# Kernel tuning notes

Measured on AMD Instinct MI355X. Metric: run time of the kernel, lower is better.

## Reference

```python
import jax, jax.numpy as jnp
import numpy as np

D_MODEL = 1024
NUM_TILES = 64
TPC = 8                 # tiles per cluster
NC = NUM_TILES // TPC   # num clusters = 8
GRID = 16
CH = D_MODEL // 4       # compress hidden = 256
EPS_LN = 1e-5


def setup_inputs() -> dict:
    key = jax.random.key(0)
    ks = jax.random.split(key, 8)
    B, T = 8, 4096
    x = jax.random.normal(ks[0], (B, T, D_MODEL), dtype=jnp.float32)
    gamma = jnp.ones((D_MODEL,), jnp.float32)
    beta = jnp.zeros((D_MODEL,), jnp.float32)
    W1 = jax.random.normal(ks[1], (CH, D_MODEL), jnp.float32) * 0.02
    b1 = jnp.zeros((CH,), jnp.float32)
    W2 = jax.random.normal(ks[2], (2, CH), jnp.float32) * 0.02
    b2 = jnp.zeros((2,), jnp.float32)
    spline_coeffs = jax.random.normal(ks[3], (NUM_TILES, GRID, GRID, 3), jnp.float32) * 0.5
    spline_scales = jnp.ones((NUM_TILES,), jnp.float32)
    directions = jax.random.normal(ks[4], (NUM_TILES, D_MODEL), jnp.float32) * 0.02
    output_scale = jnp.ones((), jnp.float32) * 0.1
    return {"x": x, "gamma": gamma, "beta": beta, "W1": W1, "b1": b1,
            "W2": W2, "b2": b2, "spline_coeffs": spline_coeffs,
            "spline_scales": spline_scales, "directions": directions,
            "output_scale": output_scale}


def _forward(x, gamma, beta, W1, b1, W2, b2, spline_coeffs, spline_scales,
             directions, output_scale):
    B, T, D = x.shape
    N = B * T
    # LayerNorm
    mu = jnp.mean(x, axis=-1, keepdims=True)
    var = jnp.mean((x - mu) ** 2, axis=-1, keepdims=True)
    x_norm = (x - mu) / jnp.sqrt(var + EPS_LN) * gamma + beta
    xf = x_norm.reshape(N, D)

    # routing signatures
    sigs = jnp.sign(directions)                                  # [NT, D]
    cluster_sigs = jnp.sign(sigs.reshape(NC, TPC, D).mean(axis=1))  # [NC, D]

    # hierarchical routing: cluster argmax then tile argmax within cluster
    cluster_idx = jnp.argmax(xf @ cluster_sigs.T, axis=-1)       # [N]
    tile_scores = (xf @ sigs.T).reshape(N, NC, TPC)              # [N, NC, TPC]
    sel = jnp.take_along_axis(tile_scores, cluster_idx[:, None, None], axis=1)[:, 0, :]
    local_idx = jnp.argmax(sel, axis=-1)                         # [N]
    tile_idx = cluster_idx * TPC + local_idx                     # cluster tiles are contiguous

    # shared compression -> (a, b) in [-1, 1]
    h = jax.nn.gelu(xf @ W1.T + b1, approximate=False)
    comp = jnp.tanh(h @ W2.T + b2)                               # [N, 2]
    a, b = comp[:, 0], comp[:, 1]

    # ternary quantized spline coefficients (STE forward value)
    q = jnp.where(spline_coeffs > 0.3, 1.0,
                  jnp.where(spline_coeffs < -0.3, -1.0, 0.0))
    qc = spline_coeffs + jax.lax.stop_gradient(q - spline_coeffs)  # [NT, G, G, 3]

    idx_a = jnp.clip(((a + 1) / 2 * GRID).astype(jnp.int32), 0, GRID - 1)
    idx_b = jnp.clip(((b + 1) / 2 * GRID).astype(jnp.int32), 0, GRID - 1)
    cell = qc[tile_idx, idx_a, idx_b]                            # [N, 3]
    cell_size = 2.0 / GRID
    local_a = (a + 1 - idx_a.astype(jnp.float32) * cell_size) / cell_size
    local_b = (b + 1 - idx_b.astype(jnp.float32) * cell_size) / cell_size
    spline_val = cell[:, 0] + cell[:, 1] * local_a + cell[:, 2] * local_b
    scale_val = spline_val * spline_scales[tile_idx]             # [N]

    out = scale_val[:, None] * directions[tile_idx]              # [N, D]
    out = out.reshape(B, T, D) * output_scale
    output = x + out                                             # dropout is identity in eval

    # load-balance aux loss
    counts = jax.ops.segment_sum(jnp.ones((N,), jnp.float32), tile_idx,
                                 num_segments=NUM_TILES)
    ideal = N / NUM_TILES
    balance = jnp.mean((counts - ideal) ** 2) / (ideal ** 2 + 1e-8) * 0.01
    return output, tile_idx.reshape(B, T), comp.reshape(B, T, 2), balance


def reference(x, gamma, beta, W1, b1, W2, b2, spline_coeffs, spline_scales,
              directions, output_scale):
    return _forward(x, gamma, beta, W1, b1, W2, b2, spline_coeffs,
                    spline_scales, directions, output_scale)
```

## Files before the change

kernel.cpp:

```cpp
#include <hip/hip_runtime.h>

#define D_MODEL 1024
#define ROWS    32
#define BT      1024
#define EPS_LN  1e-5f

typedef _Float16 f16x8 __attribute__((ext_vector_type(8)));
typedef _Float16 f16x4 __attribute__((ext_vector_type(4)));
typedef float    f32x4 __attribute__((ext_vector_type(4)));

#define WS_CNT   0
#define WS_B1P   256
#define WS_CT    1280
#define WS_FH    4096
#define WS_FL    (4096 + 688128)
#define WS_NEED  (4096 + 2 * 688128)


__global__ void prep_kernel(const float* __restrict__ W1,
                            const float* __restrict__ dirs,
                            const float* __restrict__ gamma,
                            const float* __restrict__ beta,
                            const float* __restrict__ b1,
                            char* __restrict__ wsb, int useT) {
    const int b = blockIdx.x, tid = threadIdx.x;
    if (b < 168) {
        if (!useT) return;
        const int gid = b * 256 + tid;
        const int ct = gid >> 11, ks = (gid >> 6) & 31, l = gid & 63;
        const int c16 = l & 15, kb = ks * 32 + ((l >> 4) << 3);
        f16x8 h, lo;
#pragma unroll
        for (int i = 0; i < 8; ++i) {
            const int k = kb + i;
            const float g = gamma[k];
            float v;
            if (ct < 16) {
                v = g * W1[(ct * 16 + c16) * 1024 + k];
            } else if (ct < 20) {
                const float d = dirs[((ct - 16) * 16 + c16) * 1024 + k];
                v = g * (float)((d > 0.f) - (d < 0.f));
            } else {
                if (c16 < 8) {
                    int s = 0;
                    for (int t = 0; t < 8; ++t) {
                        const float d = dirs[(c16 * 8 + t) * 1024 + k];
                        s += (d > 0.f) - (d < 0.f);
                    }
                    v = g * (float)((s > 0) - (s < 0));
                } else v = 0.f;
            }
            const _Float16 hh = (_Float16)v;
            h[i] = hh; lo[i] = (_Float16)(v - (float)hh);
        }
        *(f16x8*)(wsb + WS_FH + (size_t)gid * 16) = h;
        *(f16x8*)(wsb + WS_FL + (size_t)gid * 16) = lo;
    } else if (b < 184) {
        __shared__ float red[256];
        const int jl = tid >> 4, sub = tid & 15;
        const int j = (b - 168) * 16 + jl;
        float s = 0.f;
        for (int i = 0; i < 64; ++i) {
            const int k = sub * 64 + i;
            s += beta[k] * W1[j * 1024 + k];
        }
        red[tid] = s;
        __syncthreads();
        if (sub == 0) {
            float t = 0.f;
            for (int p = 0; p < 16; ++p) t += red[jl * 16 + p];
            ((float*)(wsb + WS_B1P))[j] = b1[j] + t;
        }
    } else if (b < 192) {
        const int t8 = (b - 184) * 8 + (tid >> 5), l32 = tid & 31;
        float s = 0.f;
        for (int i = 0; i < 32; ++i) {
            const int k = l32 * 32 + i;
            const float d = dirs[t8 * 1024 + k];
            s += beta[k] * (float)((d > 0.f) - (d < 0.f));
        }
        s += __shfl_xor(s, 1); s += __shfl_xor(s, 2); s += __shfl_xor(s, 4);
        s += __shfl_xor(s, 8); s += __shfl_xor(s, 16);
        if (l32 == 0) ((float*)(wsb + WS_CT))[t8] = s;
    } else if (b == 192) {
        const int c = tid >> 5, l32 = tid & 31;
        float s = 0.f;
        for (int i = 0; i < 32; ++i) {
            const int k = l32 * 32 + i;
            int ss = 0;
            for (int t = 0; t < 8; ++t) {
                const float d = dirs[(c * 8 + t) * 1024 + k];
                ss += (d > 0.f) - (d < 0.f);
            }
            s += beta[k] * (float)((ss > 0) - (ss < 0));
        }
        s += __shfl_xor(s, 1); s += __shfl_xor(s, 2); s += __shfl_xor(s, 4);
        s += __shfl_xor(s, 8); s += __shfl_xor(s, 16);
        if (l32 == 0) ((float*)(wsb + WS_CT))[64 + c] = s;
    } else {
        if (tid < 64) ((unsigned*)(wsb + WS_CNT))[tid] = 0u;
        else if (tid < 72) ((float*)(wsb + WS_CT))[72 + (tid - 64)] = 0.f;
    }
}

template <int USET, int NT, int CT0>
__device__ __forceinline__ void loadB(const char* __restrict__ wsb,
                                      const float* __restrict__ W1,
                                      const float* __restrict__ dirs,
                                      const float* __restrict__ gamma,
                                      int ks, int ln, f16x8* bh, f16x8* bl) {
    if (USET) {
        const size_t fo = ((size_t)((CT0 * 32 + ks) * 64 + ln)) * 16;
#pragma unroll
        for (int t = 0; t < NT; ++t) {
            bh[t] = *(const f16x8*)(wsb + WS_FH + fo + (size_t)t * 32 * 64 * 16);
            bl[t] = *(const f16x8*)(wsb + WS_FL + fo + (size_t)t * 32 * 64 * 16);
        }
    } else {
        const int c16 = ln & 15, kb = ks * 32 + ((ln >> 4) << 3);
        float g[8];
#pragma unroll
        for (int i = 0; i < 8; ++i) g[i] = gamma[kb + i];
#pragma unroll
        for (int t = 0; t < NT; ++t) {
            const int ct = CT0 + t;
#pragma unroll
            for (int i = 0; i < 8; ++i) {
                const int k = kb + i;
                float v;
                if (ct < 16) {
                    v = g[i] * W1[(ct * 16 + c16) * 1024 + k];
                } else if (ct < 20) {
                    const float d = dirs[((ct - 16) * 16 + c16) * 1024 + k];
                    v = g[i] * (float)((d > 0.f) - (d < 0.f));
                } else {
                    if (c16 < 8) {
                        int s = 0;
                        for (int tt = 0; tt < 8; ++tt) {
                            const float d = dirs[(c16 * 8 + tt) * 1024 + k];
                            s += (d > 0.f) - (d < 0.f);
                        }
                        v = g[i] * (float)((s > 0) - (s < 0));
                    } else v = 0.f;
                }
                const _Float16 hh = (_Float16)v;
                bh[t][i] = hh; bl[t][i] = (_Float16)(v - (float)hh);
            }
        }
    }
}

template <int NT>
__device__ __forceinline__ void mfma6(const f16x8 (&a)[2][2], const f16x8* bh,
                                      const f16x8* bl, f32x4 (*acc)[2]) {
    __builtin_amdgcn_s_setprio(1);
#pragma unroll
    for (int t = 0; t < NT; ++t) {
        acc[t][0] = __builtin_amdgcn_mfma_f32_16x16x32_f16(a[0][0], bh[t], acc[t][0], 0, 0, 0);
        acc[t][1] = __builtin_amdgcn_mfma_f32_16x16x32_f16(a[1][0], bh[t], acc[t][1], 0, 0, 0);
    }
#pragma unroll
    for (int t = 0; t < NT; ++t) {
        acc[t][0] = __builtin_amdgcn_mfma_f32_16x16x32_f16(a[0][0], bl[t], acc[t][0], 0, 0, 0);
        acc[t][1] = __builtin_amdgcn_mfma_f32_16x16x32_f16(a[1][0], bl[t], acc[t][1], 0, 0, 0);
    }
#pragma unroll
    for (int t = 0; t < NT; ++t) {
        acc[t][0] = __builtin_amdgcn_mfma_f32_16x16x32_f16(a[0][1], bh[t], acc[t][0], 0, 0, 0);
        acc[t][1] = __builtin_amdgcn_mfma_f32_16x16x32_f16(a[1][1], bh[t], acc[t][1], 0, 0, 0);
    }
    __builtin_amdgcn_s_setprio(0);
}

template <int USET, int NT, int CT0>
__device__ __forceinline__ void runM(const _Float16* __restrict__ xh,
                                     const _Float16* __restrict__ xl,
                                     const char* __restrict__ wsb,
                                     const float* __restrict__ W1,
                                     const float* __restrict__ dirs,
                                     const float* __restrict__ gamma,
                                     const float* __restrict__ W2,
                                     int wv, int ln,
                                     float (*scores)[84], float (*part)[32][2]) {
    const int r16 = ln & 15, kgrp = ln >> 4;
    const int kofs = kgrp << 3, asw = (r16 & 7) << 3;
    const float* b1p = (const float*)(wsb + WS_B1P);
    const float* ctv = (const float*)(wsb + WS_CT);

    f32x4 acc[NT][2];
#pragma unroll
    for (int t = 0; t < NT; ++t) {
        acc[t][0] = (f32x4){0.f, 0.f, 0.f, 0.f};
        acc[t][1] = (f32x4){0.f, 0.f, 0.f, 0.f};
    }
    f16x8 bh0[NT], bl0[NT], bh1[NT], bl1[NT];
    f16x8 a0[2][2], a1[2][2];

#define LDA2(KS, A) { const int cc_ = (((KS) * 32 + kofs) ^ asw); \
                      const int i0_ = r16 * 1024 + cc_, i1_ = (16 + r16) * 1024 + cc_; \
                      A[0][0] = *(const f16x8*)&xh[i0_]; A[0][1] = *(const f16x8*)&xl[i0_]; \
                      A[1][0] = *(const f16x8*)&xh[i1_]; A[1][1] = *(const f16x8*)&xl[i1_]; }

    loadB<USET, NT, CT0>(wsb, W1, dirs, gamma, 0, ln, bh0, bl0);
    LDA2(0, a0);
    for (int ks = 0; ks < 32; ks += 2) {
        loadB<USET, NT, CT0>(wsb, W1, dirs, gamma, ks + 1, ln, bh1, bl1);
        LDA2(ks + 1, a1);
        mfma6<NT>(a0, bh0, bl0, acc);
        if (ks + 2 < 32) {
            loadB<USET, NT, CT0>(wsb, W1, dirs, gamma, ks + 2, ln, bh0, bl0);
            LDA2(ks + 2, a0);
        }
        mfma6<NT>(a1, bh1, bl1, acc);
    }
#undef LDA2

    float p0s[2][4] = {{0.f,0.f,0.f,0.f},{0.f,0.f,0.f,0.f}};
    float p1s[2][4] = {{0.f,0.f,0.f,0.f},{0.f,0.f,0.f,0.f}};
#pragma unroll
    for (int t = 0; t < NT; ++t) {
        const int ct = CT0 + t;
        if (ct < 16) {
            const int col = ct * 16 + r16;
            const float b1c = b1p[col], w20 = W2[col], w21 = W2[256 + col];
#pragma unroll
            for (int rt = 0; rt < 2; ++rt)
#pragma unroll
                for (int reg = 0; reg < 4; ++reg) {
                    const float h = acc[t][rt][reg] + b1c;
                    const float gl = 0.5f * h * (1.f + erff(h * 0.70710678118654752f));
                    p0s[rt][reg] += gl * w20; p1s[rt][reg] += gl * w21;
                }
        } else {
            const int sc = (ct - 16) * 16 + r16;
            const float cadd = ctv[sc];
#pragma unroll
            for (int rt = 0; rt < 2; ++rt)
#pragma unroll
                for (int reg = 0; reg < 4; ++reg)
                    scores[rt * 16 + kgrp * 4 + reg][sc] = acc[t][rt][reg] + cadd;
        }
    }
    if (CT0 < 16) {
#pragma unroll
        for (int rt = 0; rt < 2; ++rt)
#pragma unroll
            for (int reg = 0; reg < 4; ++reg) {
                float v0 = p0s[rt][reg], v1 = p1s[rt][reg];
                v0 += __shfl_xor(v0, 1); v0 += __shfl_xor(v0, 2);
                v0 += __shfl_xor(v0, 4); v0 += __shfl_xor(v0, 8);
                v1 += __shfl_xor(v1, 1); v1 += __shfl_xor(v1, 2);
                v1 += __shfl_xor(v1, 4); v1 += __shfl_xor(v1, 8);
                if (r16 == 0) {
                    const int row = rt * 16 + kgrp * 4 + reg;
                    part[wv][row][0] = v0; part[wv][row][1] = v1;
                }
            }
    }
}

template <int USET>
__launch_bounds__(BT, 1)
__global__ void main_kernel(const float* __restrict__ x,
                            const float* __restrict__ gamma,
                            const float* __restrict__ beta,
                            const float* __restrict__ W1,
                            const float* __restrict__ b1,
                            const float* __restrict__ W2,
                            const float* __restrict__ b2,
                            const float* __restrict__ spline,
                            const float* __restrict__ sscale,
                            const float* __restrict__ dirs,
                            const float* __restrict__ oscale,
                            float* __restrict__ out,
                            float* __restrict__ out_tile,
                            float* __restrict__ out_comp,
                            char* __restrict__ wsb) {
    __shared__ __align__(16) _Float16 xh[ROWS * 1024];
    __shared__ __align__(16) _Float16 xl[ROWS * 1024];
    __shared__ float scores[ROWS][84];
    __shared__ float part[16][ROWS][2];
    __shared__ float mu_s[ROWS], sstd_s[ROWS];
    __shared__ float comp_ab[ROWS][2], sval_s[ROWS];
    __shared__ int   tidx_s[ROWS];

    const int tid = threadIdx.x, wv = tid >> 6, ln = tid & 63;
    const int row0 = blockIdx.x * ROWS;

    for (int q = 0; q < 2; ++q) {
        const int rl = wv * 2 + q;
        const float4* xp = (const float4*)(x + (size_t)(row0 + rl) * D_MODEL);
        float4 xv[4];
        float s = 0.f;
#pragma unroll
        for (int i = 0; i < 4; ++i) {
            xv[i] = xp[ln + 64 * i];
            s += xv[i].x + xv[i].y + xv[i].z + xv[i].w;
        }
#pragma unroll
        for (int o = 1; o < 64; o <<= 1) s += __shfl_xor(s, o);
        const float mu = s * (1.f / 1024.f);
        float v = 0.f;
#pragma unroll
        for (int i = 0; i < 4; ++i) {
            float dx;
            dx = xv[i].x - mu; v += dx * dx;
            dx = xv[i].y - mu; v += dx * dx;
            dx = xv[i].z - mu; v += dx * dx;
            dx = xv[i].w - mu; v += dx * dx;
        }
#pragma unroll
        for (int o = 1; o < 64; o <<= 1) v += __shfl_xor(v, o);
        const float sstd = sqrtf(v * (1.f / 1024.f) + EPS_LN);
        const float rstd = 1.f / sstd;
        if (ln == 0) { mu_s[rl] = mu; sstd_s[rl] = sstd; }
        const int sw = (rl & 7) << 3;
#pragma unroll
        for (int i = 0; i < 4; ++i) {
            const float o0 = (xv[i].x - mu) * rstd, o1 = (xv[i].y - mu) * rstd;
            const float o2 = (xv[i].z - mu) * rstd, o3 = (xv[i].w - mu) * rstd;
            f16x4 hv, lv;
            _Float16 t0 = (_Float16)o0; hv[0] = t0; lv[0] = (_Float16)(o0 - (float)t0);
            _Float16 t1 = (_Float16)o1; hv[1] = t1; lv[1] = (_Float16)(o1 - (float)t1);
            _Float16 t2 = (_Float16)o2; hv[2] = t2; lv[2] = (_Float16)(o2 - (float)t2);
            _Float16 t3 = (_Float16)o3; hv[3] = t3; lv[3] = (_Float16)(o3 - (float)t3);
            const int k0 = 4 * (ln + 64 * i);
            const int idx = rl * 1024 + (k0 ^ sw);
            *(f16x4*)&xh[idx] = hv;
            *(f16x4*)&xl[idx] = lv;
        }
    }
    __syncthreads();

    if (wv == 0)       runM<USET, 2, 0 >(xh, xl, wsb, W1, dirs, gamma, W2, wv, ln, scores, part);
    else if (wv == 1)  runM<USET, 2, 2 >(xh, xl, wsb, W1, dirs, gamma, W2, wv, ln, scores, part);
    else if (wv == 2)  runM<USET, 2, 4 >(xh, xl, wsb, W1, dirs, gamma, W2, wv, ln, scores, part);
    else if (wv == 3)  runM<USET, 2, 6 >(xh, xl, wsb, W1, dirs, gamma, W2, wv, ln, scores, part);
    else if (wv == 4)  runM<USET, 2, 8 >(xh, xl, wsb, W1, dirs, gamma, W2, wv, ln, scores, part);
    else if (wv == 5)  runM<USET, 1, 10>(xh, xl, wsb, W1, dirs, gamma, W2, wv, ln, scores, part);
    else if (wv == 6)  runM<USET, 1, 11>(xh, xl, wsb, W1, dirs, gamma, W2, wv, ln, scores, part);
    else if (wv == 7)  runM<USET, 1, 12>(xh, xl, wsb, W1, dirs, gamma, W2, wv, ln, scores, part);
    else if (wv == 8)  runM<USET, 1, 13>(xh, xl, wsb, W1, dirs, gamma, W2, wv, ln, scores, part);
    else if (wv == 9)  runM<USET, 1, 14>(xh, xl, wsb, W1, dirs, gamma, W2, wv, ln, scores, part);
    else if (wv == 10) runM<USET, 1, 15>(xh, xl, wsb, W1, dirs, gamma, W2, wv, ln, scores, part);
    else if (wv == 11) runM<USET, 1, 16>(xh, xl, wsb, W1, dirs, gamma, W2, wv, ln, scores, part);
    else if (wv == 12) runM<USET, 1, 17>(xh, xl, wsb, W1, dirs, gamma, W2, wv, ln, scores, part);
    else if (wv == 13) runM<USET, 1, 18>(xh, xl, wsb, W1, dirs, gamma, W2, wv, ln, scores, part);
    else if (wv == 14) runM<USET, 1, 19>(xh, xl, wsb, W1, dirs, gamma, W2, wv, ln, scores, part);
    else               runM<USET, 1, 20>(xh, xl, wsb, W1, dirs, gamma, W2, wv, ln, scores, part);
    __syncthreads();

    unsigned* cntp = (unsigned*)(wsb + WS_CNT);
    if (tid < ROWS) {
        const int r = tid;
        int bc = 0; float bs = scores[r][64];
#pragma unroll
        for (int c = 1; c < 8; ++c) { const float v = scores[r][64 + c]; if (v > bs) { bs = v; bc = c; } }
        int bt = 0; float ts = scores[r][bc * 8];
#pragma unroll
        for (int p = 1; p < 8; ++p) { const float v = scores[r][bc * 8 + p]; if (v > ts) { ts = v; bt = p; } }
        const int ti = bc * 8 + bt;
        tidx_s[r] = ti;
        atomicAdd(&cntp[ti], 1u);
        out_tile[row0 + r] = (float)ti;
    } else if (tid >= 64 && tid < 64 + 2 * ROWS) {
        const int r = (tid - 64) >> 1, cc = tid & 1;
        float s = b2[cc];
#pragma unroll
        for (int w = 0; w < 11; ++w) s += part[w][r][cc];
        s = tanhf(s);
        comp_ab[r][cc] = s;
        out_comp[(size_t)(row0 + r) * 2 + cc] = s;
    }
    __syncthreads();

    if (tid < ROWS) {
        const int r = tid;
        const float a = comp_ab[r][0], b = comp_ab[r][1];
        int ia = (int)((a + 1.0f) / 2.0f * 16.0f);
        int ib = (int)((b + 1.0f) / 2.0f * 16.0f);
        ia = min(max(ia, 0), 15); ib = min(max(ib, 0), 15);
        const int ti = tidx_s[r];
        const float* cp = spline + ((ti * 16 + ia) * 16 + ib) * 3;
        float c0 = cp[0], c1 = cp[1], c2 = cp[2];
        c0 = (c0 > 0.3f) ? 1.f : ((c0 < -0.3f) ? -1.f : 0.f);
        c1 = (c1 > 0.3f) ? 1.f : ((c1 < -0.3f) ? -1.f : 0.f);
        c2 = (c2 > 0.3f) ? 1.f : ((c2 < -0.3f) ? -1.f : 0.f);
        const float la = (a + 1.0f - (float)ia * 0.125f) * 8.0f;
        const float lb = (b + 1.0f - (float)ib * 0.125f) * 8.0f;
        sval_s[r] = (c0 + c1 * la + c2 * lb) * sscale[ti];
    }
    __syncthreads();

    const float os = oscale[0];
    for (int q = 0; q < 2; ++q) {
        const int rl = wv * 2 + q, row = row0 + rl;
        const int ti = tidx_s[rl];
        const float s = sval_s[rl] * os;
        const float mu = mu_s[rl], sd = sstd_s[rl];
        const int sw = (rl & 7) << 3;
        const float4* dp = (const float4*)(dirs + (size_t)ti * D_MODEL);
        float4* op = (float4*)(out + (size_t)row * D_MODEL);
#pragma unroll
        for (int i = 0; i < 4; ++i) {
            const int k0 = 4 * (ln + 64 * i);
            const int idx = rl * 1024 + (k0 ^ sw);
            const f16x4 hv = *(const f16x4*)&xh[idx];
            const f16x4 lv = *(const f16x4*)&xl[idx];
            const float4 dv = dp[ln + 64 * i];
            float4 o4;
            o4.x = ((float)hv[0] + (float)lv[0]) * sd + mu + s * dv.x;
            o4.y = ((float)hv[1] + (float)lv[1]) * sd + mu + s * dv.y;
            o4.z = ((float)hv[2] + (float)lv[2]) * sd + mu + s * dv.z;
            o4.w = ((float)hv[3] + (float)lv[3]) * sd + mu + s * dv.w;
            op[ln + 64 * i] = o4;
        }
    }
}

__global__ void bal_kernel(const unsigned* __restrict__ counts, float* __restrict__ ob) {
    const int t = threadIdx.x;
    const float d = (float)counts[t] - 512.0f;
    float v = d * d;
#pragma unroll
    for (int o = 1; o < 64; o <<= 1) v += __shfl_xor(v, o);
    if (t == 0) ob[0] = (v * (1.f / 64.f)) / 262144.0f * 0.01f;
}

extern "C" void kernel_launch(void* const* d_in, const int* in_sizes, int n_in,
                              void* d_out, int out_size, void* d_ws, size_t ws_size,
                              hipStream_t stream) {
    const float* x      = (const float*)d_in[0];
    const float* gamma  = (const float*)d_in[1];
    const float* beta   = (const float*)d_in[2];
    const float* W1     = (const float*)d_in[3];
    const float* b1     = (const float*)d_in[4];
    const float* W2     = (const float*)d_in[5];
    const float* b2     = (const float*)d_in[6];
    const float* spline = (const float*)d_in[7];
    const float* sscale = (const float*)d_in[8];
    const float* dirs   = (const float*)d_in[9];
    const float* oscale = (const float*)d_in[10];

    const int nrows = in_sizes[0] / D_MODEL;
    float* out      = (float*)d_out;
    float* out_tile = out + (size_t)nrows * D_MODEL;
    float* out_comp = out_tile + nrows;
    float* out_bal  = out_comp + (size_t)nrows * 2;

    char* wsb = (char*)d_ws;
    const int useT = (ws_size >= (size_t)WS_NEED) ? 1 : 0;

    prep_kernel<<<194, 256, 0, stream>>>(W1, dirs, gamma, beta, b1, wsb, useT);
    if (useT)
        main_kernel<1><<<nrows / ROWS, BT, 0, stream>>>(x, gamma, beta, W1, b1, W2, b2,
                                                        spline, sscale, dirs, oscale,
                                                        out, out_tile, out_comp, wsb);
    else
        main_kernel<0><<<nrows / ROWS, BT, 0, stream>>>(x, gamma, beta, W1, b1, W2, b2,
                                                        spline, sscale, dirs, oscale,
                                                        out, out_tile, out_comp, wsb);
    bal_kernel<<<1, 64, 0, stream>>>((const unsigned*)(wsb + WS_CNT), out_bal);
}
```

Measured before the change: 174.3 us.

## Split GEMM waves into W1 and routing-score paths, use single-precision B for signs

The fused MFMA path is split into two variants. Waves computing W1 columns keep the 3-pass split-fp16 product, while the routing-score waves use a single fp16 B operand, since sign*gamma values are exact in fp16. This cuts the score waves from six MFMAs per step to four and drops their low-part B loads. It also moves the tanh compression step into the routing thread to remove one block barrier, and widens LDS accesses in the layernorm and output phases to 8-wide fp16 vectors. The score waves were not the slowest waves (NT=2 W1 waves dominate), so the critical path may not shrink much.

```diff
diff --git a/kernel.cpp b/kernel.cpp
--- a/kernel.cpp
+++ b/kernel.cpp
@@ -6,7 +6,6 @@
 #define EPS_LN  1e-5f
 
 typedef _Float16 f16x8 __attribute__((ext_vector_type(8)));
-typedef _Float16 f16x4 __attribute__((ext_vector_type(4)));
 typedef float    f32x4 __attribute__((ext_vector_type(4)));
 
 #define WS_CNT   0
@@ -104,11 +103,10 @@
 }
 
 template <int USET, int NT, int CT0>
-__device__ __forceinline__ void loadB(const char* __restrict__ wsb,
-                                      const float* __restrict__ W1,
-                                      const float* __restrict__ dirs,
-                                      const float* __restrict__ gamma,
-                                      int ks, int ln, f16x8* bh, f16x8* bl) {
+__device__ __forceinline__ void loadBW(const char* __restrict__ wsb,
+                                       const float* __restrict__ W1,
+                                       const float* __restrict__ gamma,
+                                       int ks, int ln, f16x8* bh, f16x8* bl) {
     if (USET) {
         const size_t fo = ((size_t)((CT0 * 32 + ks) * 64 + ln)) * 16;
 #pragma unroll
@@ -118,31 +116,12 @@
         }
     } else {
         const int c16 = ln & 15, kb = ks * 32 + ((ln >> 4) << 3);
-        float g[8];
-#pragma unroll
-        for (int i = 0; i < 8; ++i) g[i] = gamma[kb + i];
 #pragma unroll
         for (int t = 0; t < NT; ++t) {
-            const int ct = CT0 + t;
 #pragma unroll
             for (int i = 0; i < 8; ++i) {
                 const int k = kb + i;
-                float v;
-                if (ct < 16) {
-                    v = g[i] * W1[(ct * 16 + c16) * 1024 + k];
-                } else if (ct < 20) {
-                    const float d = dirs[((ct - 16) * 16 + c16) * 1024 + k];
-                    v = g[i] * (float)((d > 0.f) - (d < 0.f));
-                } else {
-                    if (c16 < 8) {
-                        int s = 0;
-                        for (int tt = 0; tt < 8; ++tt) {
-                            const float d = dirs[(c16 * 8 + tt) * 1024 + k];
-                            s += (d > 0.f) - (d < 0.f);
-                        }
-                        v = g[i] * (float)((s > 0) - (s < 0));
-                    } else v = 0.f;
-                }
+                const float v = gamma[k] * W1[((CT0 + t) * 16 + c16) * 1024 + k];
                 const _Float16 hh = (_Float16)v;
                 bh[t][i] = hh; bl[t][i] = (_Float16)(v - (float)hh);
             }
@@ -150,9 +129,41 @@
     }
 }
 
+template <int USET, int CT0>
+__device__ __forceinline__ f16x8 loadBS(const char* __restrict__ wsb,
+                                        const float* __restrict__ dirs,
+                                        const float* __restrict__ gamma,
+                                        int ks, int ln) {
+    if (USET) {
+        return *(const f16x8*)(wsb + WS_FH + ((size_t)((CT0 * 32 + ks) * 64 + ln)) * 16);
+    }
+    const int c16 = ln & 15, kb = ks * 32 + ((ln >> 4) << 3);
+    f16x8 s;
+#pragma unroll
+    for (int i = 0; i < 8; ++i) {
+        const int k = kb + i;
+        float v;
+        if (CT0 < 20) {
+            const float d = dirs[((CT0 - 16) * 16 + c16) * 1024 + k];
+            v = gamma[k] * (float)((d > 0.f) - (d < 0.f));
+        } else {
+            if (c16 < 8) {
+                int ss = 0;
+                for (int tt = 0; tt < 8; ++tt) {
+                    const float d = dirs[(c16 * 8 + tt) * 1024 + k];
+                    ss += (d > 0.f) - (d < 0.f);
+                }
+                v = gamma[k] * (float)((ss > 0) - (ss < 0));
+            } else v = 0.f;
+        }
+        s[i] = (_Float16)v;
+    }
+    return s;
+}
+
 template <int NT>
-__device__ __forceinline__ void mfma6(const f16x8 (&a)[2][2], const f16x8* bh,
-                                      const f16x8* bl, f32x4 (*acc)[2]) {
+__device__ __forceinline__ void mfma3p(const f16x8 (&a)[2][2], const f16x8* bh,
+                                       const f16x8* bl, f32x4 (*acc)[2]) {
     __builtin_amdgcn_s_setprio(1);
 #pragma unroll
     for (int t = 0; t < NT; ++t) {
@@ -171,92 +182,124 @@
     }
     __builtin_amdgcn_s_setprio(0);
 }
-
-template <int USET, int NT, int CT0>
-__device__ __forceinline__ void runM(const _Float16* __restrict__ xh,
-                                     const _Float16* __restrict__ xl,
-                                     const char* __restrict__ wsb,
-                                     const float* __restrict__ W1,
-                                     const float* __restrict__ dirs,
-                                     const float* __restrict__ gamma,
-                                     const float* __restrict__ W2,
-                                     int wv, int ln,
-                                     float (*scores)[84], float (*part)[32][2]) {
-    const int r16 = ln & 15, kgrp = ln >> 4;
-    const int kofs = kgrp << 3, asw = (r16 & 7) << 3;
-    const float* b1p = (const float*)(wsb + WS_B1P);
-    const float* ctv = (const float*)(wsb + WS_CT);
-
-    f32x4 acc[NT][2];
-#pragma unroll
-    for (int t = 0; t < NT; ++t) {
-        acc[t][0] = (f32x4){0.f, 0.f, 0.f, 0.f};
-        acc[t][1] = (f32x4){0.f, 0.f, 0.f, 0.f};
-    }
-    f16x8 bh0[NT], bl0[NT], bh1[NT], bl1[NT];
-    f16x8 a0[2][2], a1[2][2];
 
 #define LDA2(KS, A) { const int cc_ = (((KS) * 32 + kofs) ^ asw); \
                       const int i0_ = r16 * 1024 + cc_, i1_ = (16 + r16) * 1024 + cc_; \
                       A[0][0] = *(const f16x8*)&xh[i0_]; A[0][1] = *(const f16x8*)&xl[i0_]; \
                       A[1][0] = *(const f16x8*)&xh[i1_]; A[1][1] = *(const f16x8*)&xl[i1_]; }
 
-    loadB<USET, NT, CT0>(wsb, W1, dirs, gamma, 0, ln, bh0, bl0);
+template <int USET, int NT, int CT0>
+__device__ __forceinline__ void runW(const _Float16* __restrict__ xh,
+                                     const _Float16* __restrict__ xl,
+                                     const char* __restrict__ wsb,
+                                     const float* __restrict__ W1,
+                                     const float* __restrict__ gamma,
+                                     const float* __restrict__ W2,
+                                     int wv, int ln, float (*part)[32][2]) {
+    const int r16 = ln & 15, kgrp = ln >> 4;
+    const int kofs = kgrp << 3, asw = (r16 & 7) << 3;
+    const float* b1p = (const float*)(wsb + WS_B1P);
+
+    f32x4 acc[NT][2];
+#pragma unroll
+    for (int t = 0; t < NT; ++t) {
+        acc[t][0] = (f32x4){0.f, 0.f, 0.f, 0.f};
+        acc[t][1] = (f32x4){0.f, 0.f, 0.f, 0.f};
+    }
+    f16x8 bh0[NT], bl0[NT], bh1[NT], bl1[NT];
+    f16x8 a0[2][2], a1[2][2];
+
+    loadBW<USET, NT, CT0>(wsb, W1, gamma, 0, ln, bh0, bl0);
     LDA2(0, a0);
     for (int ks = 0; ks < 32; ks += 2) {
-        loadB<USET, NT, CT0>(wsb, W1, dirs, gamma, ks + 1, ln, bh1, bl1);
+        loadBW<USET, NT, CT0>(wsb, W1, gamma, ks + 1, ln, bh1, bl1);
         LDA2(ks + 1, a1);
-        mfma6<NT>(a0, bh0, bl0, acc);
+        mfma3p<NT>(a0, bh0, bl0, acc);
         if (ks + 2 < 32) {
-            loadB<USET, NT, CT0>(wsb, W1, dirs, gamma, ks + 2, ln, bh0, bl0);
+            loadBW<USET, NT, CT0>(wsb, W1, gamma, ks + 2, ln, bh0, bl0);
             LDA2(ks + 2, a0);
         }
-        mfma6<NT>(a1, bh1, bl1, acc);
-    }
-#undef LDA2
+        mfma3p<NT>(a1, bh1, bl1, acc);
+    }
 
     float p0s[2][4] = {{0.f,0.f,0.f,0.f},{0.f,0.f,0.f,0.f}};
     float p1s[2][4] = {{0.f,0.f,0.f,0.f},{0.f,0.f,0.f,0.f}};
 #pragma unroll
     for (int t = 0; t < NT; ++t) {
-        const int ct = CT0 + t;
-        if (ct < 16) {
-            const int col = ct * 16 + r16;
-            const float b1c = b1p[col], w20 = W2[col], w21 = W2[256 + col];
-#pragma unroll
-            for (int rt = 0; rt < 2; ++rt)
-#pragma unroll
-                for (int reg = 0; reg < 4; ++reg) {
-                    const float h = acc[t][rt][reg] + b1c;
-                    const float gl = 0.5f * h * (1.f + erff(h * 0.70710678118654752f));
-                    p0s[rt][reg] += gl * w20; p1s[rt][reg] += gl * w21;
-                }
-        } else {
-            const int sc = (ct - 16) * 16 + r16;
-            const float cadd = ctv[sc];
-#pragma unroll
-            for (int rt = 0; rt < 2; ++rt)
-#pragma unroll
-                for (int reg = 0; reg < 4; ++reg)
-                    scores[rt * 16 + kgrp * 4 + reg][sc] = acc[t][rt][reg] + cadd;
-        }
-    }
-    if (CT0 < 16) {
+        const int col = (CT0 + t) * 16 + r16;
+        const float b1c = b1p[col], w20 = W2[col], w21 = W2[256 + col];
 #pragma unroll
         for (int rt = 0; rt < 2; ++rt)
 #pragma unroll
             for (int reg = 0; reg < 4; ++reg) {
-                float v0 = p0s[rt][reg], v1 = p1s[rt][reg];
-                v0 += __shfl_xor(v0, 1); v0 += __shfl_xor(v0, 2);
-                v0 += __shfl_xor(v0, 4); v0 += __shfl_xor(v0, 8);
-                v1 += __shfl_xor(v1, 1); v1 += __shfl_xor(v1, 2);
-                v1 += __shfl_xor(v1, 4); v1 += __shfl_xor(v1, 8);
-                if (r16 == 0) {
-                    const int row = rt * 16 + kgrp * 4 + reg;
-                    part[wv][row][0] = v0; part[wv][row][1] = v1;
-                }
-            }
-    }
+                const float h = acc[t][rt][reg] + b1c;
+                const float gl = 0.5f * h * (1.f + erff(h * 0.70710678118654752f));
+                p0s[rt][reg] += gl * w20; p1s[rt][reg] += gl * w21;
+            }
+    }
+#pragma unroll
+    for (int rt = 0; rt < 2; ++rt)
+#pragma unroll
+        for (int reg = 0; reg < 4; ++reg) {
+            float v0 = p0s[rt][reg], v1 = p1s[rt][reg];
+            v0 += __shfl_xor(v0, 1); v0 += __shfl_xor(v0, 2);
+            v0 += __shfl_xor(v0, 4); v0 += __shfl_xor(v0, 8);
+            v1 += __shfl_xor(v1, 1); v1 += __shfl_xor(v1, 2);
+            v1 += __shfl_xor(v1, 4); v1 += __shfl_xor(v1, 8);
+            if (r16 == 0) {
+                const int row = rt * 16 + kgrp * 4 + reg;
+                part[wv][row][0] = v0; part[wv][row][1] = v1;
+            }
+        }
+}
+
+template <int USET, int CT0>
+__device__ __forceinline__ void runS(const _Float16* __restrict__ xh,
+                                     const _Float16* __restrict__ xl,
+                                     const char* __restrict__ wsb,
+                                     const float* __restrict__ dirs,
+                                     const float* __restrict__ gamma,
+                                     int ln, float (*scores)[84]) {
+    const int r16 = ln & 15, kgrp = ln >> 4;
+    const int kofs = kgrp << 3, asw = (r16 & 7) << 3;
+    const float* ctv = (const float*)(wsb + WS_CT);
+
+    f32x4 acc[2];
+    acc[0] = (f32x4){0.f, 0.f, 0.f, 0.f};
+    acc[1] = (f32x4){0.f, 0.f, 0.f, 0.f};
+    f16x8 bh0, bh1;
+    f16x8 a0[2][2], a1[2][2];
+
+    bh0 = loadBS<USET, CT0>(wsb, dirs, gamma, 0, ln);
+    LDA2(0, a0);
+    for (int ks = 0; ks < 32; ks += 2) {
+        bh1 = loadBS<USET, CT0>(wsb, dirs, gamma, ks + 1, ln);
+        LDA2(ks + 1, a1);
+        __builtin_amdgcn_s_setprio(1);
+        acc[0] = __builtin_amdgcn_mfma_f32_16x16x32_f16(a0[0][0], bh0, acc[0], 0, 0, 0);
+        acc[1] = __builtin_amdgcn_mfma_f32_16x16x32_f16(a0[1][0], bh0, acc[1], 0, 0, 0);
+        acc[0] = __builtin_amdgcn_mfma_f32_16x16x32_f16(a0[0][1], bh0, acc[0], 0, 0, 0);
+        acc[1] = __builtin_amdgcn_mfma_f32_16x16x32_f16(a0[1][1], bh0, acc[1], 0, 0, 0);
+        __builtin_amdgcn_s_setprio(0);
+        if (ks + 2 < 32) {
+            bh0 = loadBS<USET, CT0>(wsb, dirs, gamma, ks + 2, ln);
+            LDA2(ks + 2, a0);
+        }
+        __builtin_amdgcn_s_setprio(1);
+        acc[0] = __builtin_amdgcn_mfma_f32_16x16x32_f16(a1[0][0], bh1, acc[0], 0, 0, 0);
+        acc[1] = __builtin_amdgcn_mfma_f32_16x16x32_f16(a1[1][0], bh1, acc[1], 0, 0, 0);
+        acc[0] = __builtin_amdgcn_mfma_f32_16x16x32_f16(a1[0][1], bh1, acc[0], 0, 0, 0);
+        acc[1] = __builtin_amdgcn_mfma_f32_16x16x32_f16(a1[1][1], bh1, acc[1], 0, 0, 0);
+        __builtin_amdgcn_s_setprio(0);
+    }
+
+    const int sc = (CT0 - 16) * 16 + r16;
+    const float cadd = ctv[sc];
+#pragma unroll
+    for (int rt = 0; rt < 2; ++rt)
+#pragma unroll
+        for (int reg = 0; reg < 4; ++reg)
+            scores[rt * 16 + kgrp * 4 + reg][sc] = acc[rt][reg] + cadd;
 }
 
 template <int USET>
@@ -279,9 +322,9 @@
     __shared__ __align__(16) _Float16 xh[ROWS * 1024];
     __shared__ __align__(16) _Float16 xl[ROWS * 1024];
     __shared__ float scores[ROWS][84];
-    __shared__ float part[16][ROWS][2];
+    __shared__ float part[11][ROWS][2];
     __shared__ float mu_s[ROWS], sstd_s[ROWS];
-    __shared__ float comp_ab[ROWS][2], sval_s[ROWS];
+    __shared__ float sval_s[ROWS];
     __shared__ int   tidx_s[ROWS];
 
     const int tid = threadIdx.x, wv = tid >> 6, ln = tid & 63;
@@ -290,25 +333,29 @@
     for (int q = 0; q < 2; ++q) {
         const int rl = wv * 2 + q;
         const float4* xp = (const float4*)(x + (size_t)(row0 + rl) * D_MODEL);
-        float4 xv[4];
+        float4 xa[2][2];
+        xa[0][0] = xp[2 * ln];       xa[0][1] = xp[2 * ln + 1];
+        xa[1][0] = xp[2 * ln + 128]; xa[1][1] = xp[2 * ln + 129];
         float s = 0.f;
 #pragma unroll
-        for (int i = 0; i < 4; ++i) {
-            xv[i] = xp[ln + 64 * i];
-            s += xv[i].x + xv[i].y + xv[i].z + xv[i].w;
-        }
+        for (int g = 0; g < 2; ++g)
+#pragma unroll
+            for (int j = 0; j < 2; ++j)
+                s += xa[g][j].x + xa[g][j].y + xa[g][j].z + xa[g][j].w;
 #pragma unroll
         for (int o = 1; o < 64; o <<= 1) s += __shfl_xor(s, o);
         const float mu = s * (1.f / 1024.f);
         float v = 0.f;
 #pragma unroll
-        for (int i = 0; i < 4; ++i) {
-            float dx;
-            dx = xv[i].x - mu; v += dx * dx;
-            dx = xv[i].y - mu; v += dx * dx;
-            dx = xv[i].z - mu; v += dx * dx;
-            dx = xv[i].w - mu; v += dx * dx;
-        }
+        for (int g = 0; g < 2; ++g)
+#pragma unroll
+            for (int j = 0; j < 2; ++j) {
+                float dx;
+                dx = xa[g][j].x - mu; v += dx * dx;
+                dx = xa[g][j].y - mu; v += dx * dx;
+                dx = xa[g][j].z - mu; v += dx * dx;
+                dx = xa[g][j].w - mu; v += dx * dx;
+            }
 #pragma unroll
         for (int o = 1; o < 64; o <<= 1) v += __shfl_xor(v, o);
         const float sstd = sqrtf(v * (1.f / 1024.f) + EPS_LN);
@@ -316,43 +363,51 @@
         if (ln == 0) { mu_s[rl] = mu; sstd_s[rl] = sstd; }
         const int sw = (rl & 7) << 3;
 #pragma unroll
-        for (int i = 0; i < 4; ++i) {
-            const float o0 = (xv[i].x - mu) * rstd, o1 = (xv[i].y - mu) * rstd;
-            const float o2 = (xv[i].z - mu) * rstd, o3 = (xv[i].w - mu) * rstd;
-            f16x4 hv, lv;
-            _Float16 t0 = (_Float16)o0; hv[0] = t0; lv[0] = (_Float16)(o0 - (float)t0);
-            _Float16 t1 = (_Float16)o1; hv[1] = t1; lv[1] = (_Float16)(o1 - (float)t1);
-            _Float16 t2 = (_Float16)o2; hv[2] = t2; lv[2] = (_Float16)(o2 - (float)t2);
-            _Float16 t3 = (_Float16)o3; hv[3] = t3; lv[3] = (_Float16)(o3 - (float)t3);
-            const int k0 = 4 * (ln + 64 * i);
-            const int idx = rl * 1024 + (k0 ^ sw);
-            *(f16x4*)&xh[idx] = hv;
-            *(f16x4*)&xl[idx] = lv;
+        for (int g = 0; g < 2; ++g) {
+            const float f[8] = {xa[g][0].x, xa[g][0].y, xa[g][0].z, xa[g][0].w,
+                                xa[g][1].x, xa[g][1].y, xa[g][1].z, xa[g][1].w};
+            f16x8 hv, lv;
+#pragma unroll
+            for (int i = 0; i < 8; ++i) {
+                const float o0 = (f[i] - mu) * rstd;
+                const _Float16 t0 = (_Float16)o0;
+                hv[i] = t0; lv[i] = (_Float16)(o0 - (float)t0);
+            }
+            const int idx = rl * 1024 + ((8 * ln + 512 * g) ^ sw);
+            *(f16x8*)&xh[idx] = hv;
+            *(f16x8*)&xl[idx] = lv;
         }
     }
     __syncthreads();
 
-    if (wv == 0)       runM<USET, 2, 0 >(xh, xl, wsb, W1, dirs, gamma, W2, wv, ln, scores, part);
-    else if (wv == 1)  runM<USET, 2, 2 >(xh, xl, wsb, W1, dirs, gamma, W2, wv, ln, scores, part);
-    else if (wv == 2)  runM<USET, 2, 4 >(xh, xl, wsb, W1, dirs, gamma, W2, wv, ln, scores, part);
-    else if (wv == 3)  runM<USET, 2, 6 >(xh, xl, wsb, W1, dirs, gamma, W2, wv, ln, scores, part);
-    else if (wv == 4)  runM<USET, 2, 8 >(xh, xl, wsb, W1, dirs, gamma, W2, wv, ln, scores, part);
-    else if (wv == 5)  runM<USET, 1, 10>(xh, xl, wsb, W1, dirs, gamma, W2, wv, ln, scores, part);
-    else if (wv == 6)  runM<USET, 1, 11>(xh, xl, wsb, W1, dirs, gamma, W2, wv, ln, scores, part);
-    else if (wv == 7)  runM<USET, 1, 12>(xh, xl, wsb, W1, dirs, gamma, W2, wv, ln, scores, part);
-    else if (wv == 8)  runM<USET, 1, 13>(xh, xl, wsb, W1, dirs, gamma, W2, wv, ln, scores, part);
-    else if (wv == 9)  runM<USET, 1, 14>(xh, xl, wsb, W1, dirs, gamma, W2, wv, ln, scores, part);
-    else if (wv == 10) runM<USET, 1, 15>(xh, xl, wsb, W1, dirs, gamma, W2, wv, ln, scores, part);
-    else if (wv == 11) runM<USET, 1, 16>(xh, xl, wsb, W1, dirs, gamma, W2, wv, ln, scores, part);
-    else if (wv == 12) runM<USET, 1, 17>(xh, xl, wsb, W1, dirs, gamma, W2, wv, ln, scores, part);
-    else if (wv == 13) runM<USET, 1, 18>(xh, xl, wsb, W1, dirs, gamma, W2, wv, ln, scores, part);
-    else if (wv == 14) runM<USET, 1, 19>(xh, xl, wsb, W1, dirs, gamma, W2, wv, ln, scores, part);
-    else               runM<USET, 1, 20>(xh, xl, wsb, W1, dirs, gamma, W2, wv, ln, scores, part);
+    if (wv == 0)       runW<USET, 2, 0 >(xh, xl, wsb, W1, gamma, W2, wv, ln, part);
+    else if (wv == 1)  runW<USET, 2, 2 >(xh, xl, wsb, W1, gamma, W2, wv, ln, part);
+    else if (wv == 2)  runW<USET, 2, 4 >(xh, xl, wsb, W1, gamma, W2, wv, ln, part);
+    else if (wv == 3)  runW<USET, 2, 6 >(xh, xl, wsb, W1, gamma, W2, wv, ln, part);
+    else if (wv == 4)  runW<USET, 2, 8 >(xh, xl, wsb, W1, gamma, W2, wv, ln, part);
+    else if (wv == 5)  runW<USET, 1, 10>(xh, xl, wsb, W1, gamma, W2, wv, ln, part);
+    else if (wv == 6)  runW<USET, 1, 11>(xh, xl, wsb, W1, gamma, W2, wv, ln, part);
+    else if (wv == 7)  runW<USET, 1, 12>(xh, xl, wsb, W1, gamma, W2, wv, ln, part);
+    else if (wv == 8)  runW<USET, 1, 13>(xh, xl, wsb, W1, gamma, W2, wv, ln, part);
+    else if (wv == 9)  runW<USET, 1, 14>(xh, xl, wsb, W1, gamma, W2, wv, ln, part);
+    else if (wv == 10) runW<USET, 1, 15>(xh, xl, wsb, W1, gamma, W2, wv, ln, part);
+    else if (wv == 11) runS<USET, 16>(xh, xl, wsb, dirs, gamma, ln, scores);
+    else if (wv == 12) runS<USET, 17>(xh, xl, wsb, dirs, gamma, ln, scores);
+    else if (wv == 13) runS<USET, 18>(xh, xl, wsb, dirs, gamma, ln, scores);
+    else if (wv == 14) runS<USET, 19>(xh, xl, wsb, dirs, gamma, ln, scores);
+    else               runS<USET, 20>(xh, xl, wsb, dirs, gamma, ln, scores);
     __syncthreads();
 
     unsigned* cntp = (unsigned*)(wsb + WS_CNT);
     if (tid < ROWS) {
         const int r = tid;
+        float c0v = b2[0], c1v = b2[1];
+#pragma unroll
+        for (int w = 0; w < 11; ++w) { c0v += part[w][r][0]; c1v += part[w][r][1]; }
+        const float a = tanhf(c0v), b = tanhf(c1v);
+        out_comp[(size_t)(row0 + r) * 2 + 0] = a;
+        out_comp[(size_t)(row0 + r) * 2 + 1] = b;
+
         int bc = 0; float bs = scores[r][64];
 #pragma unroll
         for (int c = 1; c < 8; ++c) { const float v = scores[r][64 + c]; if (v > bs) { bs = v; bc = c; } }
@@ -363,24 +418,10 @@
         tidx_s[r] = ti;
         atomicAdd(&cntp[ti], 1u);
         out_tile[row0 + r] = (float)ti;
-    } else if (tid >= 64 && tid < 64 + 2 * ROWS) {
-        const int r = (tid - 64) >> 1, cc = tid & 1;
-        float s = b2[cc];
-#pragma unroll
-        for (int w = 0; w < 11; ++w) s += part[w][r][cc];
-        s = tanhf(s);
-        comp_ab[r][cc] = s;
-        out_comp[(size_t)(row0 + r) * 2 + cc] = s;
-    }
-    __syncthreads();
-
-    if (tid < ROWS) {
-        const int r = tid;
-        const float a = comp_ab[r][0], b = comp_ab[r][1];
+
         int ia = (int)((a + 1.0f) / 2.0f * 16.0f);
         int ib = (int)((b + 1.0f) / 2.0f * 16.0f);
         ia = min(max(ia, 0), 15); ib = min(max(ib, 0), 15);
-        const int ti = tidx_s[r];
         const float* cp = spline + ((ti * 16 + ia) * 16 + ib) * 3;
         float c0 = cp[0], c1 = cp[1], c2 = cp[2];
         c0 = (c0 > 0.3f) ? 1.f : ((c0 < -0.3f) ? -1.f : 0.f);
@@ -402,18 +443,23 @@
         const float4* dp = (const float4*)(dirs + (size_t)ti * D_MODEL);
         float4* op = (float4*)(out + (size_t)row * D_MODEL);
 #pragma unroll
-        for (int i = 0; i < 4; ++i) {
-            const int k0 = 4 * (ln + 64 * i);
-            const int idx = rl * 1024 + (k0 ^ sw);
-            const f16x4 hv = *(const f16x4*)&xh[idx];
-            const f16x4 lv = *(const f16x4*)&xl[idx];
-            const float4 dv = dp[ln + 64 * i];
-            float4 o4;
-            o4.x = ((float)hv[0] + (float)lv[0]) * sd + mu + s * dv.x;
-            o4.y = ((float)hv[1] + (float)lv[1]) * sd + mu + s * dv.y;
-            o4.z = ((float)hv[2] + (float)lv[2]) * sd + mu + s * dv.z;
-            o4.w = ((float)hv[3] + (float)lv[3]) * sd + mu + s * dv.w;
-            op[ln + 64 * i] = o4;
+        for (int g = 0; g < 2; ++g) {
+            const int idx = rl * 1024 + ((8 * ln + 512 * g) ^ sw);
+            const f16x8 hv = *(const f16x8*)&xh[idx];
+            const f16x8 lv = *(const f16x8*)&xl[idx];
+            const float4 d0 = dp[2 * ln + 128 * g];
+            const float4 d1 = dp[2 * ln + 1 + 128 * g];
+            float4 o0, o1;
+            o0.x = ((float)hv[0] + (float)lv[0]) * sd + mu + s * d0.x;
+            o0.y = ((float)hv[1] + (float)lv[1]) * sd + mu + s * d0.y;
+            o0.z = ((float)hv[2] + (float)lv[2]) * sd + mu + s * d0.z;
+            o0.w = ((float)hv[3] + (float)lv[3]) * sd + mu + s * d0.w;
+            o1.x = ((float)hv[4] + (float)lv[4]) * sd + mu + s * d1.x;
+            o1.y = ((float)hv[5] + (float)lv[5]) * sd + mu + s * d1.y;
+            o1.z = ((float)hv[6] + (float)lv[6]) * sd + mu + s * d1.z;
+            o1.w = ((float)hv[7] + (float)lv[7]) * sd + mu + s * d1.w;
+            op[2 * ln + 128 * g] = o0;
+            op[2 * ln + 1 + 128 * g] = o1;
         }
     }
 }
```

New measurement: 174.2 us. No clear change (-0.1%).
